# Optimization experiments

Measured on AMD Instinct MI355X. Metric: run time of the kernel, lower is better.

Reference implementation:

```python
import jax, jax.numpy as jnp
import numpy as np

N_NODES = 50000
N_EDGES = 1600000
IN_FEATS = 256
ENC_H = 20
DEC_H = 64
BIAS = 0.0  # forward arg default
TEMPERATURE = 1.0


def setup_inputs() -> dict:
    key = jax.random.key(0)
    ks = jax.random.split(key, 8)
    x = jax.random.normal(ks[0], (N_NODES, IN_FEATS), dtype=jnp.float32)
    edge_index = jax.random.randint(ks[1], (2, N_EDGES), 0, N_NODES, dtype=jnp.int64)
    node_id = 42
    # GCNConv params (glorot-ish scale)
    W_gcn = jax.random.normal(ks[2], (IN_FEATS, ENC_H), dtype=jnp.float32) / np.sqrt(IN_FEATS)
    b_gcn = jnp.zeros((ENC_H,), dtype=jnp.float32)
    # decoder MLP params
    W1 = jax.random.normal(ks[3], (3 * ENC_H, DEC_H), dtype=jnp.float32) / np.sqrt(3 * ENC_H)
    b1 = jnp.zeros((DEC_H,), dtype=jnp.float32)
    W2 = jax.random.normal(ks[4], (DEC_H, 1), dtype=jnp.float32) / np.sqrt(DEC_H)
    b2 = jnp.zeros((1,), dtype=jnp.float32)
    return {"x": x, "edge_index": edge_index, "node_id": node_id,
            "W_gcn": W_gcn, "b_gcn": b_gcn, "W1": W1, "b1": b1, "W2": W2, "b2": b2}


def _gcn_conv(x, edge_index, W, b):
    """PyG GCNConv: add self loops, symmetric normalization, sum aggregation."""
    n = x.shape[0]
    xw = x @ W  # [N, ENC_H]
    loop = jnp.arange(n, dtype=edge_index.dtype)
    row = jnp.concatenate([edge_index[0], loop])  # source
    col = jnp.concatenate([edge_index[1], loop])  # target
    ones = jnp.ones(row.shape[0], dtype=x.dtype)
    deg = jax.ops.segment_sum(ones, col, num_segments=n)
    dinv = jnp.where(deg > 0, jax.lax.rsqrt(jnp.maximum(deg, 1e-12)), 0.0)
    norm = dinv[row] * dinv[col]  # [E+N]
    msgs = xw[row] * norm[:, None]
    out = jax.ops.segment_sum(msgs, col, num_segments=n)
    return out + b


def reference(x, edge_index, node_id, W_gcn, b_gcn, W1, b1, W2, b2):
    # encoder: GCN + ReLU
    enc = jax.nn.relu(_gcn_conv(x, edge_index, W_gcn, b_gcn))  # [N, ENC_H]
    # edge representation: [row_embed | col_embed | node_embed]
    rows, cols = edge_index[0], edge_index[1]
    node_embed = jnp.broadcast_to(enc[node_id], (rows.shape[0], enc.shape[1]))
    z = jnp.concatenate([enc[rows], enc[cols], node_embed], axis=1)  # [E, 3*ENC_H]
    # decoder MLP
    h = jax.nn.relu(z @ W1 + b1)
    out_dec = h @ W2 + b2  # [E, 1]
    # Gumbel-sigmoid sampling (training=True path)
    bias = BIAS + 0.0001
    u = jax.random.uniform(jax.random.key(123), out_dec.shape, dtype=out_dec.dtype)
    eps = (bias - (1.0 - bias)) * u + (1.0 - bias)  # in (bias, 1-bias)
    gate = jnp.log(eps) - jnp.log1p(-eps)
    return jax.nn.sigmoid((gate + out_dec) / TEMPERATURE)
```

## Files before the change

### kernel.cpp

```cpp
#include <hip/hip_runtime.h>
#include <hip/hip_bf16.h>

#define IN_FEATS 256
#define ENC_H    20
#define DEC_H    64
#define EPB      8192

__device__ __forceinline__ unsigned int rotl32(unsigned int x, int d) {
  return (x << d) | (x >> (32 - d));
}

__device__ __forceinline__ void threefry2x32(unsigned int k0, unsigned int k1,
                                             unsigned int x0, unsigned int x1,
                                             unsigned int& o0, unsigned int& o1) {
  unsigned int ks0 = k0, ks1 = k1, ks2 = k0 ^ k1 ^ 0x1BD11BDAu;
  x0 += ks0; x1 += ks1;
  x0 += x1; x1 = rotl32(x1, 13); x1 ^= x0;
  x0 += x1; x1 = rotl32(x1, 15); x1 ^= x0;
  x0 += x1; x1 = rotl32(x1, 26); x1 ^= x0;
  x0 += x1; x1 = rotl32(x1,  6); x1 ^= x0;
  x0 += ks1; x1 += ks2 + 1u;
  x0 += x1; x1 = rotl32(x1, 17); x1 ^= x0;
  x0 += x1; x1 = rotl32(x1, 29); x1 ^= x0;
  x0 += x1; x1 = rotl32(x1, 16); x1 ^= x0;
  x0 += x1; x1 = rotl32(x1, 24); x1 ^= x0;
  x0 += ks2; x1 += ks0 + 2u;
  x0 += x1; x1 = rotl32(x1, 13); x1 ^= x0;
  x0 += x1; x1 = rotl32(x1, 15); x1 ^= x0;
  x0 += x1; x1 = rotl32(x1, 26); x1 ^= x0;
  x0 += x1; x1 = rotl32(x1,  6); x1 ^= x0;
  x0 += ks0; x1 += ks1 + 3u;
  x0 += x1; x1 = rotl32(x1, 17); x1 ^= x0;
  x0 += x1; x1 = rotl32(x1, 29); x1 ^= x0;
  x0 += x1; x1 = rotl32(x1, 16); x1 ^= x0;
  x0 += x1; x1 = rotl32(x1, 24); x1 ^= x0;
  x0 += ks1; x1 += ks2 + 4u;
  x0 += x1; x1 = rotl32(x1, 13); x1 ^= x0;
  x0 += x1; x1 = rotl32(x1, 15); x1 ^= x0;
  x0 += x1; x1 = rotl32(x1, 26); x1 ^= x0;
  x0 += x1; x1 = rotl32(x1,  6); x1 ^= x0;
  x0 += ks2; x1 += ks0 + 5u;
  o0 = x0; o1 = x1;
}

__device__ __forceinline__ float2 bf2_unpack(unsigned int u) {
  float2 f;
  f.x = __uint_as_float(u << 16);
  f.y = __uint_as_float(u & 0xffff0000u);
  return f;
}


__global__ __launch_bounds__(1024) void k_binhist(const int* __restrict__ col,
                                                  int* __restrict__ bbc, int E, int nbins) {
  __shared__ int h[256];
  int t = threadIdx.x;
  if (t < 256) h[t] = 0;
  __syncthreads();
  int lo = blockIdx.x * EPB;
  int hi = min(lo + EPB, E);
  for (int e = lo + t; e < hi; e += 1024) atomicAdd(&h[col[e] >> 8], 1);
  __syncthreads();
  if (t < nbins) bbc[blockIdx.x * nbins + t] = h[t];
}

__global__ void k_colA(const int* __restrict__ bbc, int* __restrict__ base,
                       int* __restrict__ binTot, int nblk, int nbins) {
  __shared__ int sd[256];
  int t = threadIdx.x;
  int bin = blockIdx.x;
  int v = (t < nblk) ? bbc[(size_t)t * nbins + bin] : 0;
  sd[t] = v;
  __syncthreads();
#pragma unroll
  for (int off = 1; off < 256; off <<= 1) {
    int tmp = (t >= off) ? sd[t - off] : 0;
    __syncthreads();
    sd[t] += tmp;
    __syncthreads();
  }
  if (t < nblk) base[(size_t)t * nbins + bin] = sd[t] - v;
  if (t == 255) binTot[bin] = sd[255];
}

__global__ void k_colB(const int* __restrict__ binTot, int* __restrict__ binStart, int nbins) {
  __shared__ int sd[256];
  int t = threadIdx.x;
  int v = (t < nbins) ? binTot[t] : 0;
  sd[t] = v;
  __syncthreads();
#pragma unroll
  for (int off = 1; off < 256; off <<= 1) {
    int tmp = (t >= off) ? sd[t - off] : 0;
    __syncthreads();
    sd[t] += tmp;
    __syncthreads();
  }
  if (t < nbins) {
    binStart[t] = sd[t] - v;
    if (t == nbins - 1) binStart[nbins] = sd[t];
  }
}

__global__ __launch_bounds__(1024) void k_binscatter(const int* __restrict__ row,
                                                     const int* __restrict__ col,
                                                     const int* __restrict__ base,
                                                     const int* __restrict__ binStart,
                                                     unsigned int* __restrict__ binned,
                                                     int* __restrict__ einv,
                                                     int E, int nbins) {
  __shared__ int cur[256];
  int t = threadIdx.x;
  if (t < nbins) cur[t] = binStart[t] + base[(size_t)blockIdx.x * nbins + t];
  __syncthreads();
  int lo = blockIdx.x * EPB;
  int hi = min(lo + EPB, E);
  for (int e = lo + t; e < hi; e += 1024) {
    int c = col[e];
    int slot = atomicAdd(&cur[c >> 8], 1);
    binned[slot] = (unsigned int)row[e] | ((unsigned int)c << 16);
    einv[e] = slot;
  }
}

__global__ __launch_bounds__(1024) void k_binsort(const unsigned int* __restrict__ binned,
                                                  const int* __restrict__ binStart,
                                                  unsigned short* __restrict__ sorted_r,
                                                  int* __restrict__ nstart,
                                                  float* __restrict__ dinv,
                                                  int N, int E) {
  __shared__ int cnt[256];
  __shared__ int ls[256];
  __shared__ int cur[256];
  int t = threadIdx.x;
  int bin = blockIdx.x;
  if (t < 256) cnt[t] = 0;
  __syncthreads();
  int s = binStart[bin], epos = binStart[bin + 1];
  for (int i = s + t; i < epos; i += 1024)
    atomicAdd(&cnt[(binned[i] >> 16) & 0xFFu], 1);
  __syncthreads();
  int v = (t < 256) ? cnt[t] : 0;
  if (t < 256) ls[t] = v;
  __syncthreads();
#pragma unroll
  for (int off = 1; off < 256; off <<= 1) {
    int tmp = 0;
    if (t < 256 && t >= off) tmp = ls[t - off];
    __syncthreads();
    if (t < 256 && t >= off) ls[t] += tmp;
    __syncthreads();
  }
  if (t < 256) {
    int ex = ls[t] - v;
    cur[t] = s + ex;
    int n = (bin << 8) + t;
    if (n < N) {
      nstart[n] = s + ex;
      dinv[n] = rsqrtf((float)(v + 1));
    }
  }
  if (bin == 0 && t == 0) nstart[N] = E;
  __syncthreads();
  for (int i = s + t; i < epos; i += 1024) {
    unsigned int e32 = binned[i];
    int cl = (int)((e32 >> 16) & 0xFFu);
    int slot = atomicAdd(&cur[cl], 1);
    sorted_r[slot] = (unsigned short)(e32 & 0xFFFFu);
  }
}


__global__ void k_xw(const float* __restrict__ x, const float* __restrict__ W,
                     const float* __restrict__ dinv, __hip_bfloat16* __restrict__ xwd, int N) {
  __shared__ float Wl[IN_FEATS * ENC_H];
  for (int i = threadIdx.x; i < IN_FEATS * ENC_H; i += blockDim.x) Wl[i] = W[i];
  __syncthreads();
  int g = blockIdx.x * blockDim.x + threadIdx.x;
  int n = g >> 2, part = g & 3;
  if (n >= N) return;
  float acc[ENC_H];
#pragma unroll
  for (int j = 0; j < ENC_H; j++) acc[j] = 0.0f;
  const float4* x4 = reinterpret_cast<const float4*>(x + (size_t)n * IN_FEATS);
#pragma unroll 4
  for (int k4 = 0; k4 < 16; k4++) {
    float4 v = x4[k4 * 4 + part];
    int kbase = k4 * 16 + part * 4;
    const float* w0 = &Wl[(kbase + 0) * ENC_H];
    const float* w1 = &Wl[(kbase + 1) * ENC_H];
    const float* w2 = &Wl[(kbase + 2) * ENC_H];
    const float* w3 = &Wl[(kbase + 3) * ENC_H];
#pragma unroll
    for (int j = 0; j < ENC_H; j++) {
      acc[j] = fmaf(v.x, w0[j], acc[j]);
      acc[j] = fmaf(v.y, w1[j], acc[j]);
      acc[j] = fmaf(v.z, w2[j], acc[j]);
      acc[j] = fmaf(v.w, w3[j], acc[j]);
    }
  }
#pragma unroll
  for (int j = 0; j < ENC_H; j++) acc[j] += __shfl_xor(acc[j], 1);
#pragma unroll
  for (int j = 0; j < ENC_H; j++) acc[j] += __shfl_xor(acc[j], 2);
  float d = dinv[n];
  __hip_bfloat16* o = xwd + (size_t)n * ENC_H;
  int jb = part * 5;
#pragma unroll
  for (int jj = 0; jj < 5; jj++) o[jb + jj] = __float2bfloat16(acc[jb + jj] * d);
}

__global__ void k_gather(const int* __restrict__ nstart,
                         const unsigned short* __restrict__ sorted_r,
                         const __hip_bfloat16* __restrict__ xwd, const float* __restrict__ dinv,
                         const float* __restrict__ bg, float* __restrict__ enc, int N) {
  int t = blockIdx.x * blockDim.x + threadIdx.x;
  int n = t / ENC_H;
  int j = t % ENC_H;
  if (n >= N) return;
  int s = nstart[n], epos = nstart[n + 1];
  float acc = __bfloat162float(xwd[(size_t)n * ENC_H + j]);
  for (int k = s; k < epos; k++) {
    int r = (int)sorted_r[k];
    acc += __bfloat162float(xwd[(size_t)r * ENC_H + j]);
  }
  float v = acc * dinv[n] + bg[j];
  enc[(size_t)n * ENC_H + j] = fmaxf(v, 0.0f);
}

__global__ void k_pq(const float* __restrict__ enc, const float* __restrict__ W1,
                     __hip_bfloat16* __restrict__ P1, __hip_bfloat16* __restrict__ P2,
                     __hip_bfloat16* __restrict__ Q1, __hip_bfloat16* __restrict__ Q2, int N) {
  __shared__ float Wl[2 * ENC_H * DEC_H];
  for (int i = threadIdx.x; i < 2 * ENC_H * DEC_H; i += blockDim.x) Wl[i] = W1[i];
  __syncthreads();
  int t = blockIdx.x * blockDim.x + threadIdx.x;
  int n = t / DEC_H, j = t % DEC_H;
  if (n >= N) return;
  const float* en = enc + (size_t)n * ENC_H;
  float p = 0.0f, q = 0.0f;
#pragma unroll
  for (int k = 0; k < ENC_H; k++) {
    float ev = en[k];
    p = fmaf(ev, Wl[k * DEC_H + j], p);
    q = fmaf(ev, Wl[(k + ENC_H) * DEC_H + j], q);
  }
  size_t idx = (size_t)n * 32 + (j & 31);
  if (j < 32) { P1[idx] = __float2bfloat16(p); Q1[idx] = __float2bfloat16(q); }
  else        { P2[idx] = __float2bfloat16(p); Q2[idx] = __float2bfloat16(q); }
}

__global__ void k_t3(const float* __restrict__ enc, const float* __restrict__ W1,
                     const float* __restrict__ b1, const int* __restrict__ node_id,
                     float* __restrict__ t3) {
  int j = threadIdx.x;
  int nid = node_id[0];
  const float* en = enc + (size_t)nid * ENC_H;
  float a = b1[j];
#pragma unroll
  for (int k = 0; k < ENC_H; k++) a = fmaf(en[k], W1[(2 * ENC_H + k) * DEC_H + j], a);
  t3[j] = a;
}

template <int HALF>
__global__ void k_dec_half(const unsigned int* __restrict__ binned,
                           const __hip_bfloat16* __restrict__ Ph,
                           const __hip_bfloat16* __restrict__ Qh,
                           const float* __restrict__ t3, const float* __restrict__ W2,
                           const float* __restrict__ b2,
                           float* __restrict__ partial, int E) {
  __shared__ float t3l[32], w2l[32];
  if (threadIdx.x < 32) {
    t3l[threadIdx.x] = t3[HALF * 32 + threadIdx.x];
    w2l[threadIdx.x] = W2[HALF * 32 + threadIdx.x];
  }
  __syncthreads();
  int pos = blockIdx.x * blockDim.x + threadIdx.x;
  if (pos >= E) return;
  unsigned int v = binned[pos];
  int r = (int)(v & 0xFFFFu);
  int c = (int)(v >> 16);
  const uint4* pr = reinterpret_cast<const uint4*>(Ph + (size_t)r * 32);
  const uint4* qc = reinterpret_cast<const uint4*>(Qh + (size_t)c * 32);
  float acc = 0.0f;
#pragma unroll
  for (int b = 0; b < 4; b++) {
    uint4 pu = pr[b];
    uint4 qu = qc[b];
    int j0 = b * 8;
    float2 p0 = bf2_unpack(pu.x), q0 = bf2_unpack(qu.x);
    float2 p1 = bf2_unpack(pu.y), q1 = bf2_unpack(qu.y);
    float2 p2 = bf2_unpack(pu.z), q2 = bf2_unpack(qu.z);
    float2 p3 = bf2_unpack(pu.w), q3 = bf2_unpack(qu.w);
    float h;
    h = fmaxf(p0.x + q0.x + t3l[j0 + 0], 0.0f); acc = fmaf(h, w2l[j0 + 0], acc);
    h = fmaxf(p0.y + q0.y + t3l[j0 + 1], 0.0f); acc = fmaf(h, w2l[j0 + 1], acc);
    h = fmaxf(p1.x + q1.x + t3l[j0 + 2], 0.0f); acc = fmaf(h, w2l[j0 + 2], acc);
    h = fmaxf(p1.y + q1.y + t3l[j0 + 3], 0.0f); acc = fmaf(h, w2l[j0 + 3], acc);
    h = fmaxf(p2.x + q2.x + t3l[j0 + 4], 0.0f); acc = fmaf(h, w2l[j0 + 4], acc);
    h = fmaxf(p2.y + q2.y + t3l[j0 + 5], 0.0f); acc = fmaf(h, w2l[j0 + 5], acc);
    h = fmaxf(p3.x + q3.x + t3l[j0 + 6], 0.0f); acc = fmaf(h, w2l[j0 + 6], acc);
    h = fmaxf(p3.y + q3.y + t3l[j0 + 7], 0.0f); acc = fmaf(h, w2l[j0 + 7], acc);
  }
  if (HALF == 0) {
    partial[pos] = acc;
  } else {
    partial[pos] += acc + b2[0];
  }
}

__global__ void k_final(const int* __restrict__ einv, const float* __restrict__ partial,
                        float* __restrict__ out, int E) {
  int e = blockIdx.x * blockDim.x + threadIdx.x;
  if (e >= E) return;
  float od = partial[einv[e]];
  unsigned int o0, o1;
  threefry2x32(0u, 123u, 0u, (unsigned int)e, o0, o1);
  unsigned int bits = o0 ^ o1;
  float u = __uint_as_float((bits >> 9) | 0x3f800000u) - 1.0f;
  float eps = (-0.9998f) * u + 0.9999f;
  float gate = logf(eps) - log1pf(-eps);
  float s = 1.0f / (1.0f + expf(-(gate + od)));
  out[e] = s;
}

extern "C" void kernel_launch(void* const* d_in, const int* in_sizes, int n_in,
                              void* d_out, int out_size, void* d_ws, size_t ws_size,
                              hipStream_t stream) {
  const float* x       = (const float*)d_in[0];
  const int*   edge    = (const int*)d_in[1];
  const int*   node_id = (const int*)d_in[2];
  const float* W_gcn   = (const float*)d_in[3];
  const float* b_gcn   = (const float*)d_in[4];
  const float* W1      = (const float*)d_in[5];
  const float* b1      = (const float*)d_in[6];
  const float* W2      = (const float*)d_in[7];
  const float* b2      = (const float*)d_in[8];
  float* out = (float*)d_out;

  int N = in_sizes[0] / IN_FEATS;
  int E = in_sizes[1] / 2;
  const int* erow = edge;
  const int* ecol = edge + E;
  int nbins = (N + 255) >> 8;
  int NB = (E + EPB - 1) / EPB;

  char* ws = (char*)d_ws;
  size_t off = 0;
  auto alloc = [&](size_t bytes) {
    char* p = ws + off;
    off = (off + bytes + 255) & ~(size_t)255;
    return p;
  };
  __hip_bfloat16* xwd = (__hip_bfloat16*)alloc((size_t)N * ENC_H * sizeof(__hip_bfloat16));
  float* enc  = (float*)alloc((size_t)N * ENC_H * sizeof(float));
  float* dinv = (float*)alloc((size_t)N * sizeof(float));
  int*  nstart = (int*)alloc((size_t)(N + 1) * sizeof(int));
  unsigned int*   binned   = (unsigned int*)alloc((size_t)E * sizeof(unsigned int));
  int*            einv     = (int*)alloc((size_t)E * sizeof(int));
  unsigned short* sorted_r = (unsigned short*)alloc((size_t)E * sizeof(unsigned short));
  int* bbc      = (int*)alloc((size_t)NB * nbins * sizeof(int));
  int* base     = (int*)alloc((size_t)NB * nbins * sizeof(int));
  int* binTot   = (int*)alloc((size_t)nbins * sizeof(int));
  int* binStart = (int*)alloc((size_t)(nbins + 1) * sizeof(int));
  __hip_bfloat16* P1 = (__hip_bfloat16*)alloc((size_t)N * 32 * sizeof(__hip_bfloat16));
  __hip_bfloat16* P2 = (__hip_bfloat16*)alloc((size_t)N * 32 * sizeof(__hip_bfloat16));
  __hip_bfloat16* Q1 = (__hip_bfloat16*)alloc((size_t)N * 32 * sizeof(__hip_bfloat16));
  __hip_bfloat16* Q2 = (__hip_bfloat16*)alloc((size_t)N * 32 * sizeof(__hip_bfloat16));
  float* partial = (float*)alloc((size_t)E * sizeof(float));
  float* t3   = (float*)alloc((size_t)DEC_H * sizeof(float));
  (void)ws_size; (void)n_in; (void)out_size;

  const int B = 256;
  int ge  = (E + B - 1) / B;
  int gxw = (N * 4 + B - 1) / B;
  int gg  = (N * ENC_H + B - 1) / B;
  int gpq = (N * DEC_H + B - 1) / B;

  k_binhist   <<<NB, 1024, 0, stream>>>(ecol, bbc, E, nbins);
  k_colA      <<<nbins, 256, 0, stream>>>(bbc, base, binTot, NB, nbins);
  k_colB      <<<1, 256, 0, stream>>>(binTot, binStart, nbins);
  k_binscatter<<<NB, 1024, 0, stream>>>(erow, ecol, base, binStart, binned, einv, E, nbins);
  k_binsort   <<<nbins, 1024, 0, stream>>>(binned, binStart, sorted_r, nstart, dinv, N, E);
  k_xw        <<<gxw, B, 0, stream>>>(x, W_gcn, dinv, xwd, N);
  k_gather    <<<gg, B, 0, stream>>>(nstart, sorted_r, xwd, dinv, b_gcn, enc, N);
  k_pq        <<<gpq, B, 0, stream>>>(enc, W1, P1, P2, Q1, Q2, N);
  k_t3        <<<1, DEC_H, 0, stream>>>(enc, W1, b1, node_id, t3);
  k_dec_half<0><<<ge, B, 0, stream>>>(binned, P1, Q1, t3, W2, b2, partial, E);
  k_dec_half<1><<<ge, B, 0, stream>>>(binned, P2, Q2, t3, W2, b2, partial, E);
  k_final     <<<ge, B, 0, stream>>>(einv, partial, out, E);
}
```

Baseline: 187.5 us.

## Decode edges in original order with quarter-split P/Q tables, drop einv permutation

The binhist pass now writes a packed row|col word per edge in original order, and binscatter reads that packed array instead of the separate row/col inputs. The decoder now runs over edges in original order rather than in binned order, so the einv permutation array and the final gather kernel go away. The P/Q tables are split into four 16-wide quarter planes (2.5 MB each) so each pass's random-gather working set is smaller and fits better in cache. The cost is four decoder passes instead of two, each re-reading the packed edges and read-modify-writing the partial sums, and the per-edge gathers lose the locality that the binned order gave.

```diff
diff --git a/kernel.cpp b/kernel.cpp
--- a/kernel.cpp
+++ b/kernel.cpp
@@ -51,75 +51,79 @@
 }
 
 
-__global__ __launch_bounds__(1024) void k_binhist(const int* __restrict__ col,
-                                                  int* __restrict__ bbc, int E, int nbins) {
+__global__ __launch_bounds__(1024) void k_binhist(const int* __restrict__ row,
+                                                  const int* __restrict__ col,
+                                                  int* __restrict__ bbc,
+                                                  unsigned int* __restrict__ rc,
+                                                  int E, int nbins) {
   __shared__ int h[256];
   int t = threadIdx.x;
   if (t < 256) h[t] = 0;
-  __syncthreads();
-  int lo = blockIdx.x * EPB;
-  int hi = min(lo + EPB, E);
-  for (int e = lo + t; e < hi; e += 1024) atomicAdd(&h[col[e] >> 8], 1);
-  __syncthreads();
-  if (t < nbins) bbc[blockIdx.x * nbins + t] = h[t];
-}
-
-__global__ void k_colA(const int* __restrict__ bbc, int* __restrict__ base,
-                       int* __restrict__ binTot, int nblk, int nbins) {
-  __shared__ int sd[256];
-  int t = threadIdx.x;
-  int bin = blockIdx.x;
-  int v = (t < nblk) ? bbc[(size_t)t * nbins + bin] : 0;
-  sd[t] = v;
-  __syncthreads();
-#pragma unroll
-  for (int off = 1; off < 256; off <<= 1) {
-    int tmp = (t >= off) ? sd[t - off] : 0;
-    __syncthreads();
-    sd[t] += tmp;
-    __syncthreads();
-  }
-  if (t < nblk) base[(size_t)t * nbins + bin] = sd[t] - v;
-  if (t == 255) binTot[bin] = sd[255];
-}
-
-__global__ void k_colB(const int* __restrict__ binTot, int* __restrict__ binStart, int nbins) {
-  __shared__ int sd[256];
-  int t = threadIdx.x;
-  int v = (t < nbins) ? binTot[t] : 0;
-  sd[t] = v;
-  __syncthreads();
-#pragma unroll
-  for (int off = 1; off < 256; off <<= 1) {
-    int tmp = (t >= off) ? sd[t - off] : 0;
-    __syncthreads();
-    sd[t] += tmp;
-    __syncthreads();
-  }
-  if (t < nbins) {
-    binStart[t] = sd[t] - v;
-    if (t == nbins - 1) binStart[nbins] = sd[t];
-  }
-}
-
-__global__ __launch_bounds__(1024) void k_binscatter(const int* __restrict__ row,
-                                                     const int* __restrict__ col,
-                                                     const int* __restrict__ base,
-                                                     const int* __restrict__ binStart,
-                                                     unsigned int* __restrict__ binned,
-                                                     int* __restrict__ einv,
-                                                     int E, int nbins) {
-  __shared__ int cur[256];
-  int t = threadIdx.x;
-  if (t < nbins) cur[t] = binStart[t] + base[(size_t)blockIdx.x * nbins + t];
   __syncthreads();
   int lo = blockIdx.x * EPB;
   int hi = min(lo + EPB, E);
   for (int e = lo + t; e < hi; e += 1024) {
     int c = col[e];
-    int slot = atomicAdd(&cur[c >> 8], 1);
-    binned[slot] = (unsigned int)row[e] | ((unsigned int)c << 16);
-    einv[e] = slot;
+    atomicAdd(&h[c >> 8], 1);
+    rc[e] = (unsigned int)row[e] | ((unsigned int)c << 16);
+  }
+  __syncthreads();
+  if (t < nbins) bbc[blockIdx.x * nbins + t] = h[t];
+}
+
+__global__ void k_colA(const int* __restrict__ bbc, int* __restrict__ base,
+                       int* __restrict__ binTot, int nblk, int nbins) {
+  __shared__ int sd[256];
+  int t = threadIdx.x;
+  int bin = blockIdx.x;
+  int v = (t < nblk) ? bbc[(size_t)t * nbins + bin] : 0;
+  sd[t] = v;
+  __syncthreads();
+#pragma unroll
+  for (int off = 1; off < 256; off <<= 1) {
+    int tmp = (t >= off) ? sd[t - off] : 0;
+    __syncthreads();
+    sd[t] += tmp;
+    __syncthreads();
+  }
+  if (t < nblk) base[(size_t)t * nbins + bin] = sd[t] - v;
+  if (t == 255) binTot[bin] = sd[255];
+}
+
+__global__ void k_colB(const int* __restrict__ binTot, int* __restrict__ binStart, int nbins) {
+  __shared__ int sd[256];
+  int t = threadIdx.x;
+  int v = (t < nbins) ? binTot[t] : 0;
+  sd[t] = v;
+  __syncthreads();
+#pragma unroll
+  for (int off = 1; off < 256; off <<= 1) {
+    int tmp = (t >= off) ? sd[t - off] : 0;
+    __syncthreads();
+    sd[t] += tmp;
+    __syncthreads();
+  }
+  if (t < nbins) {
+    binStart[t] = sd[t] - v;
+    if (t == nbins - 1) binStart[nbins] = sd[t];
+  }
+}
+
+__global__ __launch_bounds__(1024) void k_binscatter(const unsigned int* __restrict__ rc,
+                                                     const int* __restrict__ base,
+                                                     const int* __restrict__ binStart,
+                                                     unsigned int* __restrict__ binned,
+                                                     int E, int nbins) {
+  __shared__ int cur[256];
+  int t = threadIdx.x;
+  if (t < nbins) cur[t] = binStart[t] + base[(size_t)blockIdx.x * nbins + t];
+  __syncthreads();
+  int lo = blockIdx.x * EPB;
+  int hi = min(lo + EPB, E);
+  for (int e = lo + t; e < hi; e += 1024) {
+    unsigned int v = rc[e];
+    int slot = atomicAdd(&cur[v >> 24], 1);
+    binned[slot] = v;
   }
 }
 
@@ -229,8 +233,7 @@
 }
 
 __global__ void k_pq(const float* __restrict__ enc, const float* __restrict__ W1,
-                     __hip_bfloat16* __restrict__ P1, __hip_bfloat16* __restrict__ P2,
-                     __hip_bfloat16* __restrict__ Q1, __hip_bfloat16* __restrict__ Q2, int N) {
+                     __hip_bfloat16* __restrict__ Pq, __hip_bfloat16* __restrict__ Qq, int N) {
   __shared__ float Wl[2 * ENC_H * DEC_H];
   for (int i = threadIdx.x; i < 2 * ENC_H * DEC_H; i += blockDim.x) Wl[i] = W1[i];
   __syncthreads();
@@ -245,9 +248,9 @@
     p = fmaf(ev, Wl[k * DEC_H + j], p);
     q = fmaf(ev, Wl[(k + ENC_H) * DEC_H + j], q);
   }
-  size_t idx = (size_t)n * 32 + (j & 31);
-  if (j < 32) { P1[idx] = __float2bfloat16(p); Q1[idx] = __float2bfloat16(q); }
-  else        { P2[idx] = __float2bfloat16(p); Q2[idx] = __float2bfloat16(q); }
+  size_t idx = (size_t)(j >> 4) * N * 16 + (size_t)n * 16 + (j & 15);
+  Pq[idx] = __float2bfloat16(p);
+  Qq[idx] = __float2bfloat16(q);
 }
 
 __global__ void k_t3(const float* __restrict__ enc, const float* __restrict__ W1,
@@ -262,29 +265,32 @@
   t3[j] = a;
 }
 
-template <int HALF>
-__global__ void k_dec_half(const unsigned int* __restrict__ binned,
-                           const __hip_bfloat16* __restrict__ Ph,
-                           const __hip_bfloat16* __restrict__ Qh,
-                           const float* __restrict__ t3, const float* __restrict__ W2,
-                           const float* __restrict__ b2,
-                           float* __restrict__ partial, int E) {
-  __shared__ float t3l[32], w2l[32];
-  if (threadIdx.x < 32) {
-    t3l[threadIdx.x] = t3[HALF * 32 + threadIdx.x];
-    w2l[threadIdx.x] = W2[HALF * 32 + threadIdx.x];
-  }
-  __syncthreads();
-  int pos = blockIdx.x * blockDim.x + threadIdx.x;
-  if (pos >= E) return;
-  unsigned int v = binned[pos];
+template <int Q4>
+__global__ void k_dec_q(const unsigned int* __restrict__ rc,
+                        const __hip_bfloat16* __restrict__ Pq,
+                        const __hip_bfloat16* __restrict__ Qq,
+                        const float* __restrict__ t3, const float* __restrict__ W2,
+                        const float* __restrict__ b2,
+                        float* __restrict__ partial, float* __restrict__ out,
+                        int N, int E) {
+  __shared__ float t3l[16], w2l[16];
+  if (threadIdx.x < 16) {
+    t3l[threadIdx.x] = t3[Q4 * 16 + threadIdx.x];
+    w2l[threadIdx.x] = W2[Q4 * 16 + threadIdx.x];
+  }
+  __syncthreads();
+  int e = blockIdx.x * blockDim.x + threadIdx.x;
+  if (e >= E) return;
+  unsigned int v = rc[e];
   int r = (int)(v & 0xFFFFu);
   int c = (int)(v >> 16);
-  const uint4* pr = reinterpret_cast<const uint4*>(Ph + (size_t)r * 32);
-  const uint4* qc = reinterpret_cast<const uint4*>(Qh + (size_t)c * 32);
+  const __hip_bfloat16* Pbase = Pq + (size_t)Q4 * N * 16;
+  const __hip_bfloat16* Qbase = Qq + (size_t)Q4 * N * 16;
+  const uint4* pr = reinterpret_cast<const uint4*>(Pbase + (size_t)r * 16);
+  const uint4* qc = reinterpret_cast<const uint4*>(Qbase + (size_t)c * 16);
   float acc = 0.0f;
 #pragma unroll
-  for (int b = 0; b < 4; b++) {
+  for (int b = 0; b < 2; b++) {
     uint4 pu = pr[b];
     uint4 qu = qc[b];
     int j0 = b * 8;
@@ -302,26 +308,21 @@
     h = fmaxf(p3.x + q3.x + t3l[j0 + 6], 0.0f); acc = fmaf(h, w2l[j0 + 6], acc);
     h = fmaxf(p3.y + q3.y + t3l[j0 + 7], 0.0f); acc = fmaf(h, w2l[j0 + 7], acc);
   }
-  if (HALF == 0) {
-    partial[pos] = acc;
+  if (Q4 == 0) {
+    partial[e] = acc;
+  } else if (Q4 < 3) {
+    partial[e] += acc;
   } else {
-    partial[pos] += acc + b2[0];
-  }
-}
-
-__global__ void k_final(const int* __restrict__ einv, const float* __restrict__ partial,
-                        float* __restrict__ out, int E) {
-  int e = blockIdx.x * blockDim.x + threadIdx.x;
-  if (e >= E) return;
-  float od = partial[einv[e]];
-  unsigned int o0, o1;
-  threefry2x32(0u, 123u, 0u, (unsigned int)e, o0, o1);
-  unsigned int bits = o0 ^ o1;
-  float u = __uint_as_float((bits >> 9) | 0x3f800000u) - 1.0f;
-  float eps = (-0.9998f) * u + 0.9999f;
-  float gate = logf(eps) - log1pf(-eps);
-  float s = 1.0f / (1.0f + expf(-(gate + od)));
-  out[e] = s;
+    float od = partial[e] + acc + b2[0];
+    unsigned int o0, o1;
+    threefry2x32(0u, 123u, 0u, (unsigned int)e, o0, o1);
+    unsigned int bits = o0 ^ o1;
+    float u = __uint_as_float((bits >> 9) | 0x3f800000u) - 1.0f;
+    float eps = (-0.9998f) * u + 0.9999f;
+    float gate = logf(eps) - log1pf(-eps);
+    float s = 1.0f / (1.0f + expf(-(gate + od)));
+    out[e] = s;
+  }
 }
 
 extern "C" void kernel_launch(void* const* d_in, const int* in_sizes, int n_in,
@@ -356,17 +357,15 @@
   float* enc  = (float*)alloc((size_t)N * ENC_H * sizeof(float));
   float* dinv = (float*)alloc((size_t)N * sizeof(float));
   int*  nstart = (int*)alloc((size_t)(N + 1) * sizeof(int));
+  unsigned int*   rc       = (unsigned int*)alloc((size_t)E * sizeof(unsigned int));
   unsigned int*   binned   = (unsigned int*)alloc((size_t)E * sizeof(unsigned int));
-  int*            einv     = (int*)alloc((size_t)E * sizeof(int));
   unsigned short* sorted_r = (unsigned short*)alloc((size_t)E * sizeof(unsigned short));
   int* bbc      = (int*)alloc((size_t)NB * nbins * sizeof(int));
   int* base     = (int*)alloc((size_t)NB * nbins * sizeof(int));
   int* binTot   = (int*)alloc((size_t)nbins * sizeof(int));
   int* binStart = (int*)alloc((size_t)(nbins + 1) * sizeof(int));
-  __hip_bfloat16* P1 = (__hip_bfloat16*)alloc((size_t)N * 32 * sizeof(__hip_bfloat16));
-  __hip_bfloat16* P2 = (__hip_bfloat16*)alloc((size_t)N * 32 * sizeof(__hip_bfloat16));
-  __hip_bfloat16* Q1 = (__hip_bfloat16*)alloc((size_t)N * 32 * sizeof(__hip_bfloat16));
-  __hip_bfloat16* Q2 = (__hip_bfloat16*)alloc((size_t)N * 32 * sizeof(__hip_bfloat16));
+  __hip_bfloat16* Pq = (__hip_bfloat16*)alloc((size_t)N * DEC_H * sizeof(__hip_bfloat16));
+  __hip_bfloat16* Qq = (__hip_bfloat16*)alloc((size_t)N * DEC_H * sizeof(__hip_bfloat16));
   float* partial = (float*)alloc((size_t)E * sizeof(float));
   float* t3   = (float*)alloc((size_t)DEC_H * sizeof(float));
   (void)ws_size; (void)n_in; (void)out_size;
@@ -377,16 +376,17 @@
   int gg  = (N * ENC_H + B - 1) / B;
   int gpq = (N * DEC_H + B - 1) / B;
 
-  k_binhist   <<<NB, 1024, 0, stream>>>(ecol, bbc, E, nbins);
+  k_binhist   <<<NB, 1024, 0, stream>>>(erow, ecol, bbc, rc, E, nbins);
   k_colA      <<<nbins, 256, 0, stream>>>(bbc, base, binTot, NB, nbins);
   k_colB      <<<1, 256, 0, stream>>>(binTot, binStart, nbins);
-  k_binscatter<<<NB, 1024, 0, stream>>>(erow, ecol, base, binStart, binned, einv, E, nbins);
+  k_binscatter<<<NB, 1024, 0, stream>>>(rc, base, binStart, binned, E, nbins);
   k_binsort   <<<nbins, 1024, 0, stream>>>(binned, binStart, sorted_r, nstart, dinv, N, E);
   k_xw        <<<gxw, B, 0, stream>>>(x, W_gcn, dinv, xwd, N);
   k_gather    <<<gg, B, 0, stream>>>(nstart, sorted_r, xwd, dinv, b_gcn, enc, N);
-  k_pq        <<<gpq, B, 0, stream>>>(enc, W1, P1, P2, Q1, Q2, N);
+  k_pq        <<<gpq, B, 0, stream>>>(enc, W1, Pq, Qq, N);
   k_t3        <<<1, DEC_H, 0, stream>>>(enc, W1, b1, node_id, t3);
-  k_dec_half<0><<<ge, B, 0, stream>>>(binned, P1, Q1, t3, W2, b2, partial, E);
-  k_dec_half<1><<<ge, B, 0, stream>>>(binned, P2, Q2, t3, W2, b2, partial, E);
-  k_final     <<<ge, B, 0, stream>>>(einv, partial, out, E);
-}
+  k_dec_q<0>  <<<ge, B, 0, stream>>>(rc, Pq, Qq, t3, W2, b2, partial, out, N, E);
+  k_dec_q<1>  <<<ge, B, 0, stream>>>(rc, Pq, Qq, t3, W2, b2, partial, out, N, E);
+  k_dec_q<2>  <<<ge, B, 0, stream>>>(rc, Pq, Qq, t3, W2, b2, partial, out, N, E);
+  k_dec_q<3>  <<<ge, B, 0, stream>>>(rc, Pq, Qq, t3, W2, b2, partial, out, N, E);
+}
```

Result: slower. 197.2 us (+5.2%).
